# Performance work log

Hardware: AMD Instinct MI355X
Metric: run time of the kernel (lower is better)

The kernel has to match this reference:

```python
import jax, jax.numpy as jnp
import numpy as np

HEADS = 8
D_MODEL = 512
D_K = D_MODEL // HEADS


def setup_inputs() -> dict:
    key = jax.random.key(0)
    k1, k2, k3, k4 = jax.random.split(key, 4)
    N, S = 4, 2048
    queries = jax.random.normal(k1, (N, S, D_MODEL), dtype=jnp.float32)
    keys = jax.random.normal(k2, (N, S, D_MODEL), dtype=jnp.float32)
    values = jax.random.normal(k3, (N, S, D_MODEL), dtype=jnp.float32)
    W_out = jax.random.normal(k4, (D_MODEL, D_MODEL), dtype=jnp.float32) * (1.0 / np.sqrt(D_MODEL))
    b_out = jnp.zeros((D_MODEL,), dtype=jnp.float32)
    return {"queries": queries, "keys": keys, "values": values, "W_out": W_out, "b_out": b_out}


def reference(queries, keys, values, W_out, b_out):
    N, Q, _ = queries.shape
    K = keys.shape[1]
    # NOTE: the original module defines q/k/v Linear layers but never applies
    # them in forward; inputs are reshaped directly into heads.
    q = queries.reshape(N, Q, HEADS, D_K)
    k = keys.reshape(N, K, HEADS, D_K)
    v = values.reshape(N, K, HEADS, D_K)
    # energy: [N, H, Q, K] -- full score matrix materialized, as in source
    energy = jnp.einsum('nqhd,nkhd->nhqk', q, k)
    # Quirk preserved: scale by sqrt(d_model), not sqrt(d_k)
    attn_w = jax.nn.softmax(energy / np.sqrt(D_MODEL), axis=3)
    attention = jnp.einsum('nhql,nlhd->nqhd', attn_w, v).reshape(N, Q, D_MODEL)
    # fc_output: torch Linear computes x @ W.T + b
    out = attention @ W_out.T + b_out
    return out
```

## Files before the change

### kernel.cpp

```cpp
#include <hip/hip_runtime.h>
#include <hip/hip_bf16.h>
#include <cstdint>
#include <cstddef>

#define S_LEN 2048
#define DM 512
#define DK 64

typedef __attribute__((ext_vector_type(4))) float f32x4;
typedef __attribute__((ext_vector_type(8))) short short8;

__device__ __forceinline__ unsigned short f2bf(float f) {
  union { float f; uint32_t u; } c; c.f = f;
  uint32_t u = c.u;
  u += 0x7FFF + ((u >> 16) & 1);
  return (unsigned short)(u >> 16);
}

__device__ __forceinline__ short8 ldq8(const float* p, float s) {
  float4 a = *reinterpret_cast<const float4*>(p);
  float4 b = *reinterpret_cast<const float4*>(p + 4);
  union { short8 v; unsigned int u[4]; } r;
  union { __hip_bfloat162 h; unsigned int u; } c;
  c.h = __float22bfloat162_rn(make_float2(a.x * s, a.y * s)); r.u[0] = c.u;
  c.h = __float22bfloat162_rn(make_float2(a.z * s, a.w * s)); r.u[1] = c.u;
  c.h = __float22bfloat162_rn(make_float2(b.x * s, b.y * s)); r.u[2] = c.u;
  c.h = __float22bfloat162_rn(make_float2(b.z * s, b.w * s)); r.u[3] = c.u;
  return r.v;
}

__device__ __forceinline__ void gl2lds16(const unsigned short* g, unsigned short* l) {
  __builtin_amdgcn_global_load_lds(
      (const __attribute__((address_space(1))) unsigned int*)g,
      (__attribute__((address_space(3))) unsigned int*)l, 16, 0, 0);
}

__global__ __launch_bounds__(256) void to_bf16_kernel(const float* __restrict__ in,
                                                      unsigned short* __restrict__ out,
                                                      float scale) {
  int i = (blockIdx.x * 256 + threadIdx.x) * 4;
  float4 v = *reinterpret_cast<const float4*>(in + i);
  ushort4 o;
  o.x = f2bf(v.x * scale); o.y = f2bf(v.y * scale);
  o.z = f2bf(v.z * scale); o.w = f2bf(v.w * scale);
  *reinterpret_cast<ushort4*>(out + i) = o;
}

__global__ __launch_bounds__(256) void transpose_v_kernel(const float* __restrict__ V,
                                                          unsigned short* __restrict__ Vt) {
  __shared__ unsigned short tile[64][66];
  const int lt = blockIdx.x;
  const int nh = blockIdx.y;
  const int n = nh >> 3, h = nh & 7;
  const int t = threadIdx.x;
  #pragma unroll
  for (int it = 0; it < 16; ++it) {
    int e = it * 256 + t;
    int l = e >> 6, d = e & 63;
    float v = V[((size_t)(n * S_LEN + lt * 64 + l)) * DM + h * DK + d];
    tile[l][d] = f2bf(v);
  }
  __syncthreads();
  #pragma unroll
  for (int it = 0; it < 16; ++it) {
    int e = it * 256 + t;
    int d = e >> 6, l = e & 63;
    Vt[((size_t)(nh * DK + d)) * S_LEN + lt * 64 + l] = tile[l][d];
  }
}

__global__ __launch_bounds__(128, 2) void attn_kernel(const float* __restrict__ Qf,
                                                      const unsigned short* __restrict__ Kb,
                                                      const unsigned short* __restrict__ Vt,
                                                      unsigned short* __restrict__ Ab) {
  __shared__ __align__(16) unsigned short KT[2][64 * 64];
  __shared__ __align__(16) unsigned short VT[2][64 * 64];
  __shared__ __align__(16) unsigned short PL[2][32 * 64];

  const int dlin = blockIdx.x + 32 * blockIdx.y;
  const int xcd = dlin & 7;
  const int mm = dlin >> 3;
  const int nh = xcd * 4 + (mm & 3);
  const int qt = mm >> 2;
  const int n = nh >> 3, h = nh & 7;
  const int wave = threadIdx.x >> 6;
  const int lane = threadIdx.x & 63;
  const int lr = lane & 15;
  const int lg = lane >> 4;
  const int r7 = lr & 7;

  const int q0 = qt * 64 + wave * 32;
  const float C2 = 0.063758716f;

  short8 qa[2][2];
  #pragma unroll
  for (int f = 0; f < 2; ++f) {
    const float* qp = Qf + ((size_t)(n * S_LEN + q0 + f * 16 + lr)) * DM + h * DK + lg * 8;
    qa[f][0] = ldq8(qp, C2);
    qa[f][1] = ldq8(qp + 32, C2);
  }

  f32x4 oacc[2][4];
  #pragma unroll
  for (int f = 0; f < 2; ++f)
    #pragma unroll
    for (int dt = 0; dt < 4; ++dt) oacc[f][dt] = (f32x4){0.f, 0.f, 0.f, 0.f};
  float lsum[2] = {0.f, 0.f};

  const int srow = lane >> 3;
  const int csrc = (lane & 7) ^ srow;
  const unsigned short* ksrc = Kb + ((size_t)(n * S_LEN + srow)) * DM + h * DK + csrc * 8;
  const unsigned short* vsrc = Vt + ((size_t)(nh * DK + srow)) * S_LEN + csrc * 8;
  const int kr0 = wave * 32;

#define STAGE(B_, L0_) do {                                                        \
    _Pragma("unroll")                                                              \
    for (int u = 0; u < 4; ++u)                                                    \
      gl2lds16(ksrc + (size_t)((L0_) + kr0 + u * 8) * DM, &KT[B_][(kr0 + u * 8) * 64]); \
    _Pragma("unroll")                                                              \
    for (int u = 0; u < 4; ++u)                                                    \
      gl2lds16(vsrc + (size_t)(kr0 + u * 8) * S_LEN + (L0_), &VT[B_][(kr0 + u * 8) * 64]); \
  } while (0)

#define COMPUTE(B_) do {                                                           \
    f32x4 s[4][2];                                                                 \
    _Pragma("unroll")                                                              \
    for (int nt = 0; nt < 4; ++nt) {                                               \
      const short8 kb0 = *reinterpret_cast<const short8*>(                         \
          &KT[B_][(nt * 16 + lr) * 64 + ((lg ^ r7) << 3)]);                        \
      const short8 kb1 = *reinterpret_cast<const short8*>(                         \
          &KT[B_][(nt * 16 + lr) * 64 + (((4 + lg) ^ r7) << 3)]);                  \
      _Pragma("unroll")                                                            \
      for (int f = 0; f < 2; ++f) {                                                \
        s[nt][f] = (f32x4){0.f, 0.f, 0.f, 0.f};                                    \
        s[nt][f] = __builtin_amdgcn_mfma_f32_16x16x32_bf16(kb0, qa[f][0], s[nt][f], 0, 0, 0); \
        s[nt][f] = __builtin_amdgcn_mfma_f32_16x16x32_bf16(kb1, qa[f][1], s[nt][f], 0, 0, 0); \
      }                                                                            \
    }                                                                              \
    _Pragma("unroll")                                                              \
    for (int nt = 0; nt < 4; ++nt)                                                 \
      _Pragma("unroll")                                                            \
      for (int f = 0; f < 2; ++f) {                                                \
        float p0 = __builtin_amdgcn_exp2f(s[nt][f][0]);                            \
        float p1 = __builtin_amdgcn_exp2f(s[nt][f][1]);                            \
        float p2 = __builtin_amdgcn_exp2f(s[nt][f][2]);                            \
        float p3 = __builtin_amdgcn_exp2f(s[nt][f][3]);                            \
        lsum[f] += (p0 + p1) + (p2 + p3);                                          \
        union { __hip_bfloat162 h; unsigned int u; } c0, c1;                       \
        c0.h = __float22bfloat162_rn(make_float2(p0, p1));                         \
        c1.h = __float22bfloat162_rn(make_float2(p2, p3));                         \
        uint2 w; w.x = c0.u; w.y = c1.u;                                           \
        *reinterpret_cast<uint2*>(&PL[wave][(f * 16 + lr) * 64 +                   \
            (((nt * 2 + (lg >> 1)) ^ r7) << 3) + ((lg & 1) << 2)]) = w;            \
      }                                                                            \
    _Pragma("unroll")                                                              \
    for (int kc = 0; kc < 2; ++kc) {                                               \
      const int prc = ((kc * 4 + lg) ^ r7) << 3;                                   \
      const short8 pa0 = *reinterpret_cast<const short8*>(&PL[wave][lr * 64 + prc]); \
      const short8 pa1 = *reinterpret_cast<const short8*>(&PL[wave][(16 + lr) * 64 + prc]); \
      _Pragma("unroll")                                                            \
      for (int dt = 0; dt < 4; ++dt) {                                             \
        const short8 vb = *reinterpret_cast<const short8*>(                        \
            &VT[B_][(dt * 16 + lr) * 64 + prc]);                                   \
        oacc[0][dt] = __builtin_amdgcn_mfma_f32_16x16x32_bf16(pa0, vb, oacc[0][dt], 0, 0, 0); \
        oacc[1][dt] = __builtin_amdgcn_mfma_f32_16x16x32_bf16(pa1, vb, oacc[1][dt], 0, 0, 0); \
      }                                                                            \
    }                                                                              \
  } while (0)

  STAGE(0, 0);
  asm volatile("s_waitcnt vmcnt(0)" ::: "memory");
  __syncthreads();

  for (int l0 = 0; l0 < S_LEN; l0 += 64) {
    const int cur = (l0 >> 6) & 1;
    if (l0 + 64 < S_LEN) STAGE(cur ^ 1, l0 + 64);
    COMPUTE(cur);
    __syncthreads();
  }
#undef STAGE
#undef COMPUTE

  #pragma unroll
  for (int f = 0; f < 2; ++f) {
    lsum[f] += __shfl_xor(lsum[f], 16);
    lsum[f] += __shfl_xor(lsum[f], 32);
  }

  unsigned short* ab = Ab + ((size_t)(n * S_LEN + q0)) * DM + h * DK + lr;
  #pragma unroll
  for (int f = 0; f < 2; ++f)
    #pragma unroll
    for (int j = 0; j < 4; ++j) {
      float rl = 1.f / __shfl(lsum[f], lg * 4 + j);
      #pragma unroll
      for (int dt = 0; dt < 4; ++dt)
        ab[(size_t)(f * 16 + lg * 4 + j) * DM + dt * 16] = f2bf(oacc[f][dt][j] * rl);
    }
}

__global__ __launch_bounds__(256, 2) void proj_kernel(const unsigned short* __restrict__ Ab,
                                                      const unsigned short* __restrict__ Wb,
                                                      const float* __restrict__ bias,
                                                      float* __restrict__ out) {
  __shared__ __align__(16) unsigned short At[2][128 * 64];
  __shared__ __align__(16) unsigned short Wt[2][64 * 64];

  const int m0 = blockIdx.x * 128;
  const int o0 = blockIdx.y * 64;
  const int wave = threadIdx.x >> 6;
  const int lane = threadIdx.x & 63;
  const int lr = lane & 15;
  const int lg = lane >> 4;
  const int r7 = lr & 7;
  const int wm = (wave >> 1) * 64;
  const int wn = (wave & 1) * 32;

  const int srow = lane >> 3;
  const int csrc = (lane & 7) ^ srow;
  const unsigned short* asrc = Ab + ((size_t)(m0 + wave * 32 + srow)) * DM + csrc * 8;
  const unsigned short* wsrc = Wb + ((size_t)(o0 + wave * 16 + srow)) * DM + csrc * 8;

  float bv[2];
  #pragma unroll
  for (int nf = 0; nf < 2; ++nf) bv[nf] = bias[o0 + wn + nf * 16 + lr];

  f32x4 acc[4][2];
  #pragma unroll
  for (int mf = 0; mf < 4; ++mf)
    #pragma unroll
    for (int nf = 0; nf < 2; ++nf) acc[mf][nf] = (f32x4){0.f, 0.f, 0.f, 0.f};

#define PSTAGE(B_, KB_) do {                                                       \
    _Pragma("unroll")                                                              \
    for (int u = 0; u < 4; ++u)                                                    \
      gl2lds16(asrc + (size_t)(u * 8) * DM + (KB_), &At[B_][(wave * 32 + u * 8) * 64]); \
    _Pragma("unroll")                                                              \
    for (int u = 0; u < 2; ++u)                                                    \
      gl2lds16(wsrc + (size_t)(u * 8) * DM + (KB_), &Wt[B_][(wave * 16 + u * 8) * 64]); \
  } while (0)

#define PCOMPUTE(B_) do {                                                          \
    _Pragma("unroll")                                                              \
    for (int kc = 0; kc < 2; ++kc) {                                               \
      const int sw = ((kc * 4 + lg) ^ r7) << 3;                                    \
      short8 af[4], wf[2];                                                         \
      _Pragma("unroll")                                                            \
      for (int mf = 0; mf < 4; ++mf)                                               \
        af[mf] = *reinterpret_cast<const short8*>(&At[B_][(wm + mf * 16 + lr) * 64 + sw]); \
      _Pragma("unroll")                                                            \
      for (int nf = 0; nf < 2; ++nf)                                               \
        wf[nf] = *reinterpret_cast<const short8*>(&Wt[B_][(wn + nf * 16 + lr) * 64 + sw]); \
      _Pragma("unroll")                                                            \
      for (int mf = 0; mf < 4; ++mf)                                               \
        _Pragma("unroll")                                                          \
        for (int nf = 0; nf < 2; ++nf)                                             \
          acc[mf][nf] = __builtin_amdgcn_mfma_f32_16x16x32_bf16(af[mf], wf[nf], acc[mf][nf], 0, 0, 0); \
    }                                                                              \
  } while (0)

  PSTAGE(0, 0);
  asm volatile("s_waitcnt vmcnt(0)" ::: "memory");
  __syncthreads();

  for (int kb = 0; kb < DM; kb += 64) {
    const int cur = (kb >> 6) & 1;
    if (kb + 64 < DM) PSTAGE(cur ^ 1, kb + 64);
    PCOMPUTE(cur);
    __syncthreads();
  }
#undef PSTAGE
#undef PCOMPUTE

  #pragma unroll
  for (int mf = 0; mf < 4; ++mf) {
    #pragma unroll
    for (int j = 0; j < 4; ++j) {
      float* op = out + (size_t)(m0 + wm + mf * 16 + lg * 4 + j) * DM + o0 + wn + lr;
      #pragma unroll
      for (int nf = 0; nf < 2; ++nf)
        op[nf * 16] = acc[mf][nf][j] + bv[nf];
    }
  }
}

extern "C" void kernel_launch(void* const* d_in, const int* in_sizes, int n_in,
                              void* d_out, int out_size, void* d_ws, size_t ws_size,
                              hipStream_t stream) {
  const float* Q = (const float*)d_in[0];
  const float* K = (const float*)d_in[1];
  const float* V = (const float*)d_in[2];
  const float* W = (const float*)d_in[3];
  const float* b = (const float*)d_in[4];
  float* out = (float*)d_out;

  char* ws = (char*)d_ws;
  unsigned short* Kb = (unsigned short*)(ws);
  unsigned short* Vt = (unsigned short*)(ws + 8388608);
  unsigned short* Ab = (unsigned short*)(ws + 16777216);
  unsigned short* Wb = (unsigned short*)(ws + 25165824);

  to_bf16_kernel<<<4096, 256, 0, stream>>>(K, Kb, 1.0f);
  to_bf16_kernel<<<256, 256, 0, stream>>>(W, Wb, 1.0f);
  transpose_v_kernel<<<dim3(32, 32), 256, 0, stream>>>(V, Vt);
  attn_kernel<<<dim3(32, 32), 128, 0, stream>>>(Q, Kb, Vt, Ab);
  proj_kernel<<<dim3(64, 8), 256, 0, stream>>>(Ab, Wb, b, out);
}
```

Before: 82.35 us.

## Switch attention to 32x32x16 MFMA and keep probabilities in registers via permlane swap

Rewrites the attention inner loop to use 32x32x16 bf16 MFMA tiles instead of 16x16x32, computing scores transposed (K rows by query columns) so each lane owns one query row. The exponentiated probabilities are packed to bf16 and rearranged with v_permlane32_swap, so they feed the PV MFMA directly from registers. This removes the per-wave LDS staging buffer for P and its write/read round trip. It also simplifies the row-sum reduction and output store. The trade-offs are larger accumulator register usage and reliance on a gfx950-specific permlane instruction.

After: 85.86 us. 1.04x slower.

```diff
diff --git a/kernel.cpp b/kernel.cpp
--- a/kernel.cpp
+++ b/kernel.cpp
@@ -8,6 +8,7 @@
 #define DK 64
 
 typedef __attribute__((ext_vector_type(4))) float f32x4;
+typedef __attribute__((ext_vector_type(16))) float f32x16;
 typedef __attribute__((ext_vector_type(8))) short short8;
 
 __device__ __forceinline__ unsigned short f2bf(float f) {
@@ -17,15 +18,20 @@
   return (unsigned short)(u >> 16);
 }
 
+__device__ __forceinline__ unsigned int pkbf(float a, float b) {
+  union { __hip_bfloat162 h; unsigned int u; } c;
+  c.h = __float22bfloat162_rn(make_float2(a, b));
+  return c.u;
+}
+
 __device__ __forceinline__ short8 ldq8(const float* p, float s) {
   float4 a = *reinterpret_cast<const float4*>(p);
   float4 b = *reinterpret_cast<const float4*>(p + 4);
   union { short8 v; unsigned int u[4]; } r;
-  union { __hip_bfloat162 h; unsigned int u; } c;
-  c.h = __float22bfloat162_rn(make_float2(a.x * s, a.y * s)); r.u[0] = c.u;
-  c.h = __float22bfloat162_rn(make_float2(a.z * s, a.w * s)); r.u[1] = c.u;
-  c.h = __float22bfloat162_rn(make_float2(b.x * s, b.y * s)); r.u[2] = c.u;
-  c.h = __float22bfloat162_rn(make_float2(b.z * s, b.w * s)); r.u[3] = c.u;
+  r.u[0] = pkbf(a.x * s, a.y * s);
+  r.u[1] = pkbf(a.z * s, a.w * s);
+  r.u[2] = pkbf(b.x * s, b.y * s);
+  r.u[3] = pkbf(b.z * s, b.w * s);
   return r.v;
 }
 
@@ -34,6 +40,8 @@
       (const __attribute__((address_space(1))) unsigned int*)g,
       (__attribute__((address_space(3))) unsigned int*)l, 16, 0, 0);
 }
+
+#define SWAP32(a, b) asm volatile("v_permlane32_swap_b32 %0, %1" : "+v"(a), "+v"(b))
 
 __global__ __launch_bounds__(256) void to_bf16_kernel(const float* __restrict__ in,
                                                       unsigned short* __restrict__ out,
@@ -75,7 +83,6 @@
                                                       unsigned short* __restrict__ Ab) {
   __shared__ __align__(16) unsigned short KT[2][64 * 64];
   __shared__ __align__(16) unsigned short VT[2][64 * 64];
-  __shared__ __align__(16) unsigned short PL[2][32 * 64];
 
   const int dlin = blockIdx.x + 32 * blockIdx.y;
   const int xcd = dlin & 7;
@@ -85,27 +92,22 @@
   const int n = nh >> 3, h = nh & 7;
   const int wave = threadIdx.x >> 6;
   const int lane = threadIdx.x & 63;
-  const int lr = lane & 15;
-  const int lg = lane >> 4;
-  const int r7 = lr & 7;
+  const int l31 = lane & 31;
+  const int hi = lane >> 5;
+  const int r7 = l31 & 7;
 
   const int q0 = qt * 64 + wave * 32;
   const float C2 = 0.063758716f;
 
-  short8 qa[2][2];
-  #pragma unroll
-  for (int f = 0; f < 2; ++f) {
-    const float* qp = Qf + ((size_t)(n * S_LEN + q0 + f * 16 + lr)) * DM + h * DK + lg * 8;
-    qa[f][0] = ldq8(qp, C2);
-    qa[f][1] = ldq8(qp + 32, C2);
-  }
-
-  f32x4 oacc[2][4];
-  #pragma unroll
-  for (int f = 0; f < 2; ++f)
-    #pragma unroll
-    for (int dt = 0; dt < 4; ++dt) oacc[f][dt] = (f32x4){0.f, 0.f, 0.f, 0.f};
-  float lsum[2] = {0.f, 0.f};
+  short8 qa[4];
+  const float* qp = Qf + ((size_t)(n * S_LEN + q0 + l31)) * DM + h * DK + hi * 8;
+  #pragma unroll
+  for (int ks = 0; ks < 4; ++ks) qa[ks] = ldq8(qp + ks * 16, C2);
+
+  f32x16 oacc0, oacc1;
+  #pragma unroll
+  for (int i = 0; i < 16; ++i) { oacc0[i] = 0.f; oacc1[i] = 0.f; }
+  float lsum = 0.f;
 
   const int srow = lane >> 3;
   const int csrc = (lane & 7) ^ srow;
@@ -122,49 +124,44 @@
       gl2lds16(vsrc + (size_t)(kr0 + u * 8) * S_LEN + (L0_), &VT[B_][(kr0 + u * 8) * 64]); \
   } while (0)
 
+#define SM32(S_, C0_, C1_) do {                                                    \
+    float p[16];                                                                   \
+    _Pragma("unroll")                                                              \
+    for (int i = 0; i < 16; ++i) p[i] = __builtin_amdgcn_exp2f(S_[i]);             \
+    lsum += (((p[0] + p[1]) + (p[2] + p[3])) + ((p[4] + p[5]) + (p[6] + p[7])))    \
+          + (((p[8] + p[9]) + (p[10] + p[11])) + ((p[12] + p[13]) + (p[14] + p[15]))); \
+    unsigned int x0 = pkbf(p[0], p[1]),   x1 = pkbf(p[2], p[3]);                   \
+    unsigned int y0 = pkbf(p[4], p[5]),   y1 = pkbf(p[6], p[7]);                   \
+    unsigned int x2 = pkbf(p[8], p[9]),   x3 = pkbf(p[10], p[11]);                 \
+    unsigned int y2 = pkbf(p[12], p[13]), y3 = pkbf(p[14], p[15]);                 \
+    SWAP32(x0, y0); SWAP32(x1, y1); SWAP32(x2, y2); SWAP32(x3, y3);                \
+    C0_.u[0] = x0; C0_.u[1] = x1; C0_.u[2] = y0; C0_.u[3] = y1;                    \
+    C1_.u[0] = x2; C1_.u[1] = x3; C1_.u[2] = y2; C1_.u[3] = y3;                    \
+  } while (0)
+
 #define COMPUTE(B_) do {                                                           \
-    f32x4 s[4][2];                                                                 \
-    _Pragma("unroll")                                                              \
-    for (int nt = 0; nt < 4; ++nt) {                                               \
-      const short8 kb0 = *reinterpret_cast<const short8*>(                         \
-          &KT[B_][(nt * 16 + lr) * 64 + ((lg ^ r7) << 3)]);                        \
-      const short8 kb1 = *reinterpret_cast<const short8*>(                         \
-          &KT[B_][(nt * 16 + lr) * 64 + (((4 + lg) ^ r7) << 3)]);                  \
-      _Pragma("unroll")                                                            \
-      for (int f = 0; f < 2; ++f) {                                                \
-        s[nt][f] = (f32x4){0.f, 0.f, 0.f, 0.f};                                    \
-        s[nt][f] = __builtin_amdgcn_mfma_f32_16x16x32_bf16(kb0, qa[f][0], s[nt][f], 0, 0, 0); \
-        s[nt][f] = __builtin_amdgcn_mfma_f32_16x16x32_bf16(kb1, qa[f][1], s[nt][f], 0, 0, 0); \
-      }                                                                            \
+    f32x16 s0, s1;                                                                 \
+    _Pragma("unroll")                                                              \
+    for (int i = 0; i < 16; ++i) { s0[i] = 0.f; s1[i] = 0.f; }                     \
+    _Pragma("unroll")                                                              \
+    for (int ks = 0; ks < 4; ++ks) {                                               \
+      const int kchunk = (((ks * 2 + hi) ^ r7) << 3);                              \
+      const short8 k0 = *reinterpret_cast<const short8*>(&KT[B_][l31 * 64 + kchunk]); \
+      const short8 k1 = *reinterpret_cast<const short8*>(&KT[B_][(32 + l31) * 64 + kchunk]); \
+      s0 = __builtin_amdgcn_mfma_f32_32x32x16_bf16(k0, qa[ks], s0, 0, 0, 0);       \
+      s1 = __builtin_amdgcn_mfma_f32_32x32x16_bf16(k1, qa[ks], s1, 0, 0, 0);       \
     }                                                                              \
-    _Pragma("unroll")                                                              \
-    for (int nt = 0; nt < 4; ++nt)                                                 \
-      _Pragma("unroll")                                                            \
-      for (int f = 0; f < 2; ++f) {                                                \
-        float p0 = __builtin_amdgcn_exp2f(s[nt][f][0]);                            \
-        float p1 = __builtin_amdgcn_exp2f(s[nt][f][1]);                            \
-        float p2 = __builtin_amdgcn_exp2f(s[nt][f][2]);                            \
-        float p3 = __builtin_amdgcn_exp2f(s[nt][f][3]);                            \
-        lsum[f] += (p0 + p1) + (p2 + p3);                                          \
-        union { __hip_bfloat162 h; unsigned int u; } c0, c1;                       \
-        c0.h = __float22bfloat162_rn(make_float2(p0, p1));                         \
-        c1.h = __float22bfloat162_rn(make_float2(p2, p3));                         \
-        uint2 w; w.x = c0.u; w.y = c1.u;                                           \
-        *reinterpret_cast<uint2*>(&PL[wave][(f * 16 + lr) * 64 +                   \
-            (((nt * 2 + (lg >> 1)) ^ r7) << 3) + ((lg & 1) << 2)]) = w;            \
-      }                                                                            \
-    _Pragma("unroll")                                                              \
-    for (int kc = 0; kc < 2; ++kc) {                                               \
-      const int prc = ((kc * 4 + lg) ^ r7) << 3;                                   \
-      const short8 pa0 = *reinterpret_cast<const short8*>(&PL[wave][lr * 64 + prc]); \
-      const short8 pa1 = *reinterpret_cast<const short8*>(&PL[wave][(16 + lr) * 64 + prc]); \
-      _Pragma("unroll")                                                            \
-      for (int dt = 0; dt < 4; ++dt) {                                             \
-        const short8 vb = *reinterpret_cast<const short8*>(                        \
-            &VT[B_][(dt * 16 + lr) * 64 + prc]);                                   \
-        oacc[0][dt] = __builtin_amdgcn_mfma_f32_16x16x32_bf16(pa0, vb, oacc[0][dt], 0, 0, 0); \
-        oacc[1][dt] = __builtin_amdgcn_mfma_f32_16x16x32_bf16(pa1, vb, oacc[1][dt], 0, 0, 0); \
-      }                                                                            \
+    union { short8 v; unsigned int u[4]; } pb0, pb1, pb2, pb3;                     \
+    SM32(s0, pb0, pb1);                                                            \
+    SM32(s1, pb2, pb3);                                                            \
+    _Pragma("unroll")                                                              \
+    for (int c = 0; c < 4; ++c) {                                                  \
+      const int vchunk = (((c * 2 + hi) ^ r7) << 3);                               \
+      const short8 v0 = *reinterpret_cast<const short8*>(&VT[B_][l31 * 64 + vchunk]); \
+      const short8 v1 = *reinterpret_cast<const short8*>(&VT[B_][(32 + l31) * 64 + vchunk]); \
+      const short8 pv = (c == 0) ? pb0.v : (c == 1) ? pb1.v : (c == 2) ? pb2.v : pb3.v; \
+      oacc0 = __builtin_amdgcn_mfma_f32_32x32x16_bf16(v0, pv, oacc0, 0, 0, 0);     \
+      oacc1 = __builtin_amdgcn_mfma_f32_32x32x16_bf16(v1, pv, oacc1, 0, 0, 0);     \
     }                                                                              \
   } while (0)
 
@@ -180,23 +177,22 @@
   }
 #undef STAGE
 #undef COMPUTE
-
-  #pragma unroll
-  for (int f = 0; f < 2; ++f) {
-    lsum[f] += __shfl_xor(lsum[f], 16);
-    lsum[f] += __shfl_xor(lsum[f], 32);
-  }
-
-  unsigned short* ab = Ab + ((size_t)(n * S_LEN + q0)) * DM + h * DK + lr;
-  #pragma unroll
-  for (int f = 0; f < 2; ++f)
-    #pragma unroll
-    for (int j = 0; j < 4; ++j) {
-      float rl = 1.f / __shfl(lsum[f], lg * 4 + j);
-      #pragma unroll
-      for (int dt = 0; dt < 4; ++dt)
-        ab[(size_t)(f * 16 + lg * 4 + j) * DM + dt * 16] = f2bf(oacc[f][dt][j] * rl);
-    }
+#undef SM32
+
+  lsum += __shfl_xor(lsum, 32);
+  const float rl = 1.f / lsum;
+
+  unsigned short* ab = Ab + ((size_t)(n * S_LEN + q0 + l31)) * DM + h * DK + hi * 4;
+  #pragma unroll
+  for (int g = 0; g < 4; ++g) {
+    uint2 w0, w1;
+    w0.x = pkbf(oacc0[4 * g] * rl, oacc0[4 * g + 1] * rl);
+    w0.y = pkbf(oacc0[4 * g + 2] * rl, oacc0[4 * g + 3] * rl);
+    *reinterpret_cast<uint2*>(ab + g * 8) = w0;
+    w1.x = pkbf(oacc1[4 * g] * rl, oacc1[4 * g + 1] * rl);
+    w1.y = pkbf(oacc1[4 * g + 2] * rl, oacc1[4 * g + 3] * rl);
+    *reinterpret_cast<uint2*>(ab + 32 + g * 8) = w1;
+  }
 }
 
 __global__ __launch_bounds__(256, 2) void proj_kernel(const unsigned short* __restrict__ Ab,
```

## Double per-wave query rows in attention and fuse prep kernels into one launch

Applied to the files above, without the earlier changes.

The attention kernel now gives each wave 64 query rows instead of 32 and each block 128 query rows, halving the grid to 512 blocks. Each K/V tile loaded into LDS is therefore reused across twice as many MFMAs, which cuts global and LDS traffic per unit of work. The cost is more accumulator registers, lower occupancy (launch bounds drop to 1 block per CU) and fewer blocks across the 256 CUs. Separately, the K conversion, W conversion and V transpose kernels are merged into one prep launch to save launch overhead.

After: 104.3 us. 1.27x slower.

```diff
diff --git a/kernel.cpp b/kernel.cpp
--- a/kernel.cpp
+++ b/kernel.cpp
@@ -17,15 +17,20 @@
   return (unsigned short)(u >> 16);
 }
 
+__device__ __forceinline__ unsigned int pkbf(float a, float b) {
+  union { __hip_bfloat162 h; unsigned int u; } c;
+  c.h = __float22bfloat162_rn(make_float2(a, b));
+  return c.u;
+}
+
 __device__ __forceinline__ short8 ldq8(const float* p, float s) {
   float4 a = *reinterpret_cast<const float4*>(p);
   float4 b = *reinterpret_cast<const float4*>(p + 4);
   union { short8 v; unsigned int u[4]; } r;
-  union { __hip_bfloat162 h; unsigned int u; } c;
-  c.h = __float22bfloat162_rn(make_float2(a.x * s, a.y * s)); r.u[0] = c.u;
-  c.h = __float22bfloat162_rn(make_float2(a.z * s, a.w * s)); r.u[1] = c.u;
-  c.h = __float22bfloat162_rn(make_float2(b.x * s, b.y * s)); r.u[2] = c.u;
-  c.h = __float22bfloat162_rn(make_float2(b.z * s, b.w * s)); r.u[3] = c.u;
+  r.u[0] = pkbf(a.x * s, a.y * s);
+  r.u[1] = pkbf(a.z * s, a.w * s);
+  r.u[2] = pkbf(b.x * s, b.y * s);
+  r.u[3] = pkbf(b.z * s, b.w * s);
   return r.v;
 }
 
@@ -35,53 +40,62 @@
       (__attribute__((address_space(3))) unsigned int*)l, 16, 0, 0);
 }
 
-__global__ __launch_bounds__(256) void to_bf16_kernel(const float* __restrict__ in,
-                                                      unsigned short* __restrict__ out,
-                                                      float scale) {
-  int i = (blockIdx.x * 256 + threadIdx.x) * 4;
-  float4 v = *reinterpret_cast<const float4*>(in + i);
-  ushort4 o;
-  o.x = f2bf(v.x * scale); o.y = f2bf(v.y * scale);
-  o.z = f2bf(v.z * scale); o.w = f2bf(v.w * scale);
-  *reinterpret_cast<ushort4*>(out + i) = o;
-}
-
-__global__ __launch_bounds__(256) void transpose_v_kernel(const float* __restrict__ V,
-                                                          unsigned short* __restrict__ Vt) {
+__global__ __launch_bounds__(256) void prep_kernel(const float* __restrict__ K,
+                                                   const float* __restrict__ V,
+                                                   const float* __restrict__ W,
+                                                   unsigned short* __restrict__ Kb,
+                                                   unsigned short* __restrict__ Vt,
+                                                   unsigned short* __restrict__ Wb) {
   __shared__ unsigned short tile[64][66];
-  const int lt = blockIdx.x;
-  const int nh = blockIdx.y;
-  const int n = nh >> 3, h = nh & 7;
+  const int bid = blockIdx.x;
   const int t = threadIdx.x;
-  #pragma unroll
-  for (int it = 0; it < 16; ++it) {
-    int e = it * 256 + t;
-    int l = e >> 6, d = e & 63;
-    float v = V[((size_t)(n * S_LEN + lt * 64 + l)) * DM + h * DK + d];
-    tile[l][d] = f2bf(v);
-  }
-  __syncthreads();
-  #pragma unroll
-  for (int it = 0; it < 16; ++it) {
-    int e = it * 256 + t;
-    int d = e >> 6, l = e & 63;
-    Vt[((size_t)(nh * DK + d)) * S_LEN + lt * 64 + l] = tile[l][d];
-  }
-}
-
-__global__ __launch_bounds__(128, 2) void attn_kernel(const float* __restrict__ Qf,
+  if (bid < 4096) {
+    int i = (bid * 256 + t) * 4;
+    float4 v = *reinterpret_cast<const float4*>(K + i);
+    ushort4 o;
+    o.x = f2bf(v.x); o.y = f2bf(v.y); o.z = f2bf(v.z); o.w = f2bf(v.w);
+    *reinterpret_cast<ushort4*>(Kb + i) = o;
+  } else if (bid < 4352) {
+    int i = ((bid - 4096) * 256 + t) * 4;
+    float4 v = *reinterpret_cast<const float4*>(W + i);
+    ushort4 o;
+    o.x = f2bf(v.x); o.y = f2bf(v.y); o.z = f2bf(v.z); o.w = f2bf(v.w);
+    *reinterpret_cast<ushort4*>(Wb + i) = o;
+  } else {
+    const int r = bid - 4352;
+    const int lt = r & 31;
+    const int nh = r >> 5;
+    const int n = nh >> 3, h = nh & 7;
+    #pragma unroll
+    for (int it = 0; it < 16; ++it) {
+      int e = it * 256 + t;
+      int l = e >> 6, d = e & 63;
+      float v = V[((size_t)(n * S_LEN + lt * 64 + l)) * DM + h * DK + d];
+      tile[l][d] = f2bf(v);
+    }
+    __syncthreads();
+    #pragma unroll
+    for (int it = 0; it < 16; ++it) {
+      int e = it * 256 + t;
+      int d = e >> 6, l = e & 63;
+      Vt[((size_t)(nh * DK + d)) * S_LEN + lt * 64 + l] = tile[l][d];
+    }
+  }
+}
+
+__global__ __launch_bounds__(128, 1) void attn_kernel(const float* __restrict__ Qf,
                                                       const unsigned short* __restrict__ Kb,
                                                       const unsigned short* __restrict__ Vt,
                                                       unsigned short* __restrict__ Ab) {
   __shared__ __align__(16) unsigned short KT[2][64 * 64];
   __shared__ __align__(16) unsigned short VT[2][64 * 64];
-  __shared__ __align__(16) unsigned short PL[2][32 * 64];
-
-  const int dlin = blockIdx.x + 32 * blockIdx.y;
+  __shared__ __align__(16) unsigned short PL[2][64 * 64];
+
+  const int dlin = blockIdx.x + 16 * blockIdx.y;
   const int xcd = dlin & 7;
   const int mm = dlin >> 3;
   const int nh = xcd * 4 + (mm & 3);
-  const int qt = mm >> 2;
+  const int qsb = mm >> 2;
   const int n = nh >> 3, h = nh & 7;
   const int wave = threadIdx.x >> 6;
   const int lane = threadIdx.x & 63;
@@ -89,23 +103,23 @@
   const int lg = lane >> 4;
   const int r7 = lr & 7;
 
-  const int q0 = qt * 64 + wave * 32;
+  const int q0 = qsb * 128 + wave * 64;
   const float C2 = 0.063758716f;
 
-  short8 qa[2][2];
-  #pragma unroll
-  for (int f = 0; f < 2; ++f) {
+  short8 qa[4][2];
+  #pragma unroll
+  for (int f = 0; f < 4; ++f) {
     const float* qp = Qf + ((size_t)(n * S_LEN + q0 + f * 16 + lr)) * DM + h * DK + lg * 8;
     qa[f][0] = ldq8(qp, C2);
     qa[f][1] = ldq8(qp + 32, C2);
   }
 
-  f32x4 oacc[2][4];
-  #pragma unroll
-  for (int f = 0; f < 2; ++f)
+  f32x4 oacc[4][4];
+  #pragma unroll
+  for (int f = 0; f < 4; ++f)
     #pragma unroll
     for (int dt = 0; dt < 4; ++dt) oacc[f][dt] = (f32x4){0.f, 0.f, 0.f, 0.f};
-  float lsum[2] = {0.f, 0.f};
+  float lsum[4] = {0.f, 0.f, 0.f, 0.f};
 
   const int srow = lane >> 3;
   const int csrc = (lane & 7) ^ srow;
@@ -123,7 +137,7 @@
   } while (0)
 
 #define COMPUTE(B_) do {                                                           \
-    f32x4 s[4][2];                                                                 \
+    f32x4 s[4][4];                                                                 \
     _Pragma("unroll")                                                              \
     for (int nt = 0; nt < 4; ++nt) {                                               \
       const short8 kb0 = *reinterpret_cast<const short8*>(                         \
@@ -131,7 +145,7 @@
       const short8 kb1 = *reinterpret_cast<const short8*>(                         \
           &KT[B_][(nt * 16 + lr) * 64 + (((4 + lg) ^ r7) << 3)]);                  \
       _Pragma("unroll")                                                            \
-      for (int f = 0; f < 2; ++f) {                                                \
+      for (int f = 0; f < 4; ++f) {                                                \
         s[nt][f] = (f32x4){0.f, 0.f, 0.f, 0.f};                                    \
         s[nt][f] = __builtin_amdgcn_mfma_f32_16x16x32_bf16(kb0, qa[f][0], s[nt][f], 0, 0, 0); \
         s[nt][f] = __builtin_amdgcn_mfma_f32_16x16x32_bf16(kb1, qa[f][1], s[nt][f], 0, 0, 0); \
@@ -140,30 +154,30 @@
     _Pragma("unroll")                                                              \
     for (int nt = 0; nt < 4; ++nt)                                                 \
       _Pragma("unroll")                                                            \
-      for (int f = 0; f < 2; ++f) {                                                \
+      for (int f = 0; f < 4; ++f) {                                                \
         float p0 = __builtin_amdgcn_exp2f(s[nt][f][0]);                            \
         float p1 = __builtin_amdgcn_exp2f(s[nt][f][1]);                            \
         float p2 = __builtin_amdgcn_exp2f(s[nt][f][2]);                            \
         float p3 = __builtin_amdgcn_exp2f(s[nt][f][3]);                            \
         lsum[f] += (p0 + p1) + (p2 + p3);                                          \
-        union { __hip_bfloat162 h; unsigned int u; } c0, c1;                       \
-        c0.h = __float22bfloat162_rn(make_float2(p0, p1));                         \
-        c1.h = __float22bfloat162_rn(make_float2(p2, p3));                         \
-        uint2 w; w.x = c0.u; w.y = c1.u;                                           \
+        uint2 w; w.x = pkbf(p0, p1); w.y = pkbf(p2, p3);                           \
         *reinterpret_cast<uint2*>(&PL[wave][(f * 16 + lr) * 64 +                   \
             (((nt * 2 + (lg >> 1)) ^ r7) << 3) + ((lg & 1) << 2)]) = w;            \
       }                                                                            \
     _Pragma("unroll")                                                              \
     for (int kc = 0; kc < 2; ++kc) {                                               \
       const int prc = ((kc * 4 + lg) ^ r7) << 3;                                   \
-      const short8 pa0 = *reinterpret_cast<const short8*>(&PL[wave][lr * 64 + prc]); \
-      const short8 pa1 = *reinterpret_cast<const short8*>(&PL[wave][(16 + lr) * 64 + prc]); \
+      short8 pa[4];                                                                \
+      _Pragma("unroll")                                                            \
+      for (int f = 0; f < 4; ++f)                                                  \
+        pa[f] = *reinterpret_cast<const short8*>(&PL[wave][(f * 16 + lr) * 64 + prc]); \
       _Pragma("unroll")                                                            \
       for (int dt = 0; dt < 4; ++dt) {                                             \
         const short8 vb = *reinterpret_cast<const short8*>(                        \
             &VT[B_][(dt * 16 + lr) * 64 + prc]);                                   \
-        oacc[0][dt] = __builtin_amdgcn_mfma_f32_16x16x32_bf16(pa0, vb, oacc[0][dt], 0, 0, 0); \
-        oacc[1][dt] = __builtin_amdgcn_mfma_f32_16x16x32_bf16(pa1, vb, oacc[1][dt], 0, 0, 0); \
+        _Pragma("unroll")                                                          \
+        for (int f = 0; f < 4; ++f)                                                \
+          oacc[f][dt] = __builtin_amdgcn_mfma_f32_16x16x32_bf16(pa[f], vb, oacc[f][dt], 0, 0, 0); \
       }                                                                            \
     }                                                                              \
   } while (0)
@@ -182,14 +196,14 @@
 #undef COMPUTE
 
   #pragma unroll
-  for (int f = 0; f < 2; ++f) {
+  for (int f = 0; f < 4; ++f) {
     lsum[f] += __shfl_xor(lsum[f], 16);
     lsum[f] += __shfl_xor(lsum[f], 32);
   }
 
   unsigned short* ab = Ab + ((size_t)(n * S_LEN + q0)) * DM + h * DK + lr;
   #pragma unroll
-  for (int f = 0; f < 2; ++f)
+  for (int f = 0; f < 4; ++f)
     #pragma unroll
     for (int j = 0; j < 4; ++j) {
       float rl = 1.f / __shfl(lsum[f], lg * 4 + j);
@@ -300,9 +314,7 @@
   unsigned short* Ab = (unsigned short*)(ws + 16777216);
   unsigned short* Wb = (unsigned short*)(ws + 25165824);
 
-  to_bf16_kernel<<<4096, 256, 0, stream>>>(K, Kb, 1.0f);
-  to_bf16_kernel<<<256, 256, 0, stream>>>(W, Wb, 1.0f);
-  transpose_v_kernel<<<dim3(32, 32), 256, 0, stream>>>(V, Vt);
-  attn_kernel<<<dim3(32, 32), 128, 0, stream>>>(Q, Kb, Vt, Ab);
+  prep_kernel<<<5376, 256, 0, stream>>>(K, V, W, Kb, Vt, Wb);
+  attn_kernel<<<dim3(16, 32), 128, 0, stream>>>(Q, Kb, Vt, Ab);
   proj_kernel<<<dim3(64, 8), 256, 0, stream>>>(Ab, Wb, b, out);
 }
```
